# Performance work log

Hardware: AMD Instinct MI355X
Metric: run time of the kernel (lower is better)

The kernel has to match this reference:

```python
import jax, jax.numpy as jnp
import numpy as np
from jax import lax

D_MODEL = 1024
D_STATE = 16
D_CONV = 4
D_INNER = 2048  # expand * d_model
DT_RANK = 64    # ceil(d_model / 16)
BATCH = 2
SEQ = 2048


def setup_inputs() -> dict:
    key = jax.random.key(0)
    ks = jax.random.split(key, 8)
    s = 0.02
    x = jax.random.normal(ks[0], (BATCH, SEQ, D_MODEL), jnp.float32)
    in_proj_w = jax.random.normal(ks[1], (2 * D_INNER, D_MODEL), jnp.float32) * s
    conv_w = jax.random.normal(ks[2], (D_INNER, 1, D_CONV), jnp.float32) * s  # [out, in/groups, k]
    conv_b = jax.random.normal(ks[3], (D_INNER,), jnp.float32) * s
    x_proj_w = jax.random.normal(ks[4], (DT_RANK + 2 * D_STATE, D_INNER), jnp.float32) * s
    dt_proj_w = jax.random.normal(ks[5], (D_INNER, DT_RANK), jnp.float32) * s
    dt_proj_b = jax.random.normal(ks[6], (D_INNER,), jnp.float32) * s
    A_log = jnp.log(jnp.tile(jnp.arange(1, D_STATE + 1, dtype=jnp.float32), (D_INNER, 1)))
    D = jnp.ones((D_INNER,), jnp.float32)
    out_proj_w = jax.random.normal(ks[7], (D_MODEL, D_INNER), jnp.float32) * s
    return dict(x=x, in_proj_w=in_proj_w, conv_w=conv_w, conv_b=conv_b,
                x_proj_w=x_proj_w, dt_proj_w=dt_proj_w, dt_proj_b=dt_proj_b,
                A_log=A_log, D=D, out_proj_w=out_proj_w)


def _causal_depthwise_conv(x_bcl, conv_w, conv_b):
    # x_bcl: [B, d_inner, L]; conv_w: [d_inner, 1, k]; left-pad k-1 -> causal, output length L
    y = lax.conv_general_dilated(
        x_bcl, conv_w,
        window_strides=(1,), padding=[(D_CONV - 1, 0)],
        feature_group_count=D_INNER,
        dimension_numbers=('NCH', 'OIH', 'NCH'))
    return y + conv_b[None, :, None]


def _ssm(xc, x_proj_w, dt_proj_w, dt_proj_b, A_log, D):
    # xc: [B, L, d_inner]
    A = -jnp.exp(A_log)                                   # [d, N]
    x_dbl = jnp.einsum('bld,rd->blr', xc, x_proj_w)       # [B, L, dt_rank + 2N]
    dt_low = x_dbl[..., :DT_RANK]
    Bm = x_dbl[..., DT_RANK:DT_RANK + D_STATE]            # [B, L, N]
    Cm = x_dbl[..., DT_RANK + D_STATE:]                   # [B, L, N]
    dt = jax.nn.softplus(jnp.einsum('blr,dr->bld', dt_low, dt_proj_w) + dt_proj_b)  # [B, L, d]
    dA = jnp.exp(dt[..., None] * A)                       # [B, L, d, N]
    dBx = dt[..., None] * Bm[:, :, None, :] * xc[..., None]  # [B, L, d, N]

    def step(h, inp):
        dA_t, dBx_t, C_t = inp                            # [B,d,N], [B,d,N], [B,N]
        h = dA_t * h + dBx_t
        y = jnp.einsum('bdn,bn->bd', h, C_t)
        return h, y

    h0 = jnp.zeros((xc.shape[0], D_INNER, D_STATE), xc.dtype)
    _, ys = lax.scan(step, h0,
                     (dA.transpose(1, 0, 2, 3), dBx.transpose(1, 0, 2, 3), Cm.transpose(1, 0, 2)))
    y = ys.transpose(1, 0, 2)                             # [B, L, d]
    return y + xc * D


def reference(x, in_proj_w, conv_w, conv_b, x_proj_w, dt_proj_w, dt_proj_b, A_log, D, out_proj_w):
    xz = jnp.einsum('blm,om->blo', x, in_proj_w)          # [B, L, 2*d_inner]
    xs, z = jnp.split(xz, 2, axis=-1)
    xc = _causal_depthwise_conv(xs.transpose(0, 2, 1), conv_w, conv_b).transpose(0, 2, 1)
    xc = jax.nn.silu(xc)
    y = _ssm(xc, x_proj_w, dt_proj_w, dt_proj_b, A_log, D)
    out = y * jax.nn.silu(z)
    return jnp.einsum('bld,md->blm', out, out_proj_w)
```

## Files before the change

### kernel.cpp

```cpp
#include <hip/hip_runtime.h>

#define SEQ    2048
#define DIN    2048
#define DMODEL 1024
#define NROWS  4096
#define NCH    32
#define CHL    64

typedef __attribute__((ext_vector_type(8))) _Float16 half8v;
typedef __attribute__((ext_vector_type(4))) float f32x4;

__device__ __forceinline__ float sigf(float x) { return 1.0f / (1.0f + __expf(-x)); }
__device__ __forceinline__ float softplusf(float v) {
    return fmaxf(v, 0.f) + __logf(1.f + __expf(-fabsf(v)));
}

__device__ __forceinline__ float* deadp(float* xzbuf, size_t j) {
    return xzbuf + ((j >> 11) << 12) + (j & 2047);
}
__device__ __forceinline__ float* deadp2(float* xzbuf, size_t j) {
    return xzbuf + ((size_t)(2048 + (j >> 11)) << 12) + (j & 2047);
}

__device__ __forceinline__ void gload16(const void* g, const void* l) {
    __builtin_amdgcn_global_load_lds((const __attribute__((address_space(1))) void*)g,
                                     (__attribute__((address_space(3))) void*)l, 16, 0, 0);
}

__device__ __forceinline__ unsigned short f2h(float x) {
    _Float16 h = (_Float16)x;
    unsigned short u;
    __builtin_memcpy(&u, &h, 2);
    return u;
}
__device__ __forceinline__ float h2f(unsigned short u) {
    _Float16 h;
    __builtin_memcpy(&h, &u, 2);
    return (float)h;
}

__global__ __launch_bounds__(256) void cvt_in_k(
    const float* __restrict__ x, const float* __restrict__ wi, const float* __restrict__ wx,
    unsigned short* __restrict__ xh, unsigned short* __restrict__ wih,
    unsigned short* __restrict__ wxh)
{
    int i = blockIdx.x * 256 + threadIdx.x;
    if (i < 1048576) {
        float4 v = ((const float4*)x)[i];
        ushort4 h; h.x = f2h(v.x); h.y = f2h(v.y); h.z = f2h(v.z); h.w = f2h(v.w);
        ((ushort4*)xh)[i] = h;
    } else if (i < 2097152) {
        i -= 1048576;
        float4 v = ((const float4*)wi)[i];
        ushort4 h; h.x = f2h(v.x); h.y = f2h(v.y); h.z = f2h(v.z); h.w = f2h(v.w);
        ((ushort4*)wih)[i] = h;
    } else if (i < 2162688) {
        i -= 2097152;
        int row = i >> 9, q = i & 511;
        ushort4 h;
        if (row < 96) {
            float4 v = ((const float4*)wx)[(size_t)row * 512 + q];
            h.x = f2h(v.x); h.y = f2h(v.y); h.z = f2h(v.z); h.w = f2h(v.w);
        } else h = make_ushort4(0, 0, 0, 0);
        ((ushort4*)wxh)[(size_t)row * 512 + q] = h;
    }
}

__global__ __launch_bounds__(256) void cvt_dt_k(
    const float* __restrict__ xdbl, const float* __restrict__ wd, const float* __restrict__ wo,
    unsigned short* __restrict__ dlh, unsigned short* __restrict__ wdh,
    unsigned short* __restrict__ woh)
{
    int i = blockIdx.x * 256 + threadIdx.x;
    if (i < 65536) {
        int row = i >> 4, q = i & 15;
        float4 v = *(const float4*)(xdbl + (size_t)row * 96 + q * 4);
        ushort4 h; h.x = f2h(v.x); h.y = f2h(v.y); h.z = f2h(v.z); h.w = f2h(v.w);
        *(ushort4*)(dlh + (size_t)row * 8192 + q * 4) = h;
    } else if (i < 98304) {
        i -= 65536;
        int row = i >> 4, q = i & 15;
        float4 v = *(const float4*)(wd + (size_t)row * 64 + q * 4);
        ushort4 h; h.x = f2h(v.x); h.y = f2h(v.y); h.z = f2h(v.z); h.w = f2h(v.w);
        *(ushort4*)(wdh + (size_t)row * 8192 + q * 4) = h;
    } else if (i < 622592) {
        i -= 98304;
        float4 v = ((const float4*)wo)[i];
        ushort4 h; h.x = f2h(v.x); h.y = f2h(v.y); h.z = f2h(v.z); h.w = f2h(v.w);
        ((ushort4*)woh)[i] = h;
    }
}

__global__ __launch_bounds__(512, 2) void gemm256_h(
    const unsigned short* __restrict__ A, const unsigned short* __restrict__ W,
    float* __restrict__ C, int K, int N, int mtiles, int lda, int ldw)
{
    __shared__ uint4 ldsu4[8192];
    char* lds = (char*)ldsu4;
    const int tid = threadIdx.x;
    const int w = tid >> 6, lane = tid & 63;

    const int nwg = gridDim.x;
    const int cpx = nwg >> 3;
    const int bid = blockIdx.x;
    const int swz = (bid & 7) * cpx + (bid >> 3);
    const int ntiles = nwg / mtiles;
    const int per = 8 * ntiles;
    const int gid = swz / per;
    const int rem = swz - gid * per;
    const int m0 = (gid * 8 + (rem & 7)) * 256;
    const int n0 = (rem >> 3) * 256;

    const int wr = w >> 2, wc = w & 3;
    const int lm = lane & 15, lk = lane >> 4;

    f32x4 acc[8][4];
#pragma unroll
    for (int i = 0; i < 8; ++i)
#pragma unroll
        for (int j = 0; j < 4; ++j) { acc[i][j][0]=0.f; acc[i][j][1]=0.f; acc[i][j][2]=0.f; acc[i][j][3]=0.f; }

    const int rsub = w * 8 + (lane >> 3);
    const int xr8  = ((lane & 7) ^ (lane >> 3)) << 3;
    const unsigned short* gA = A + (size_t)(m0 + rsub) * lda + xr8;
    const unsigned short* gW = W + (size_t)(n0 + rsub) * ldw + xr8;
    const int sdst = w * 1024;

    auto stageA = [&](int bb, int hi, int kt) {
        char* d = lds + bb * 65536 + hi * 16384 + sdst;
        const unsigned short* s = gA + (size_t)hi * 128 * lda + kt;
        gload16(s, d);
        gload16(s + (size_t)64 * lda, d + 8192);
    };
    auto stageB = [&](int bb, int hi, int kt) {
        char* d = lds + bb * 65536 + 32768 + hi * 16384 + sdst;
        const unsigned short* s = gW + (size_t)hi * 128 * ldw + kt;
        gload16(s, d);
        gload16(s + (size_t)64 * ldw, d + 8192);
    };

    half8v a[4][2], b[2][2][2];
    auto loadA = [&](int bb, int mh) {
#pragma unroll
        for (int mb = 0; mb < 4; ++mb)
#pragma unroll
            for (int kk = 0; kk < 2; ++kk) {
                int ar = wr * 128 + (mh * 4 + mb) * 16 + lm;
                a[mb][kk] = *(const half8v*)(lds + bb * 65536 + ar * 128 + (((kk * 4 + lk) ^ (lm & 7)) << 4));
            }
    };
    auto loadB = [&](int bb, int nh) {
#pragma unroll
        for (int nb = 0; nb < 2; ++nb)
#pragma unroll
            for (int kk = 0; kk < 2; ++kk) {
                int br = wc * 64 + (nh * 2 + nb) * 16 + lm;
                b[nh][nb][kk] = *(const half8v*)(lds + bb * 65536 + 32768 + br * 128 + (((kk * 4 + lk) ^ (lm & 7)) << 4));
            }
    };
    auto mm = [&](int mh, int nh) {
        __builtin_amdgcn_s_setprio(1);
#pragma unroll
        for (int mb = 0; mb < 4; ++mb)
#pragma unroll
            for (int nb = 0; nb < 2; ++nb)
#pragma unroll
                for (int kk = 0; kk < 2; ++kk)
                    acc[mh * 4 + mb][nh * 2 + nb] = __builtin_amdgcn_mfma_f32_16x16x32_f16(
                        a[mb][kk], b[nh][nb][kk], acc[mh * 4 + mb][nh * 2 + nb], 0, 0, 0);
        __builtin_amdgcn_s_setprio(0);
    };
#define VMW4() asm volatile("s_waitcnt vmcnt(4)" ::: "memory")
#define BAR()  __builtin_amdgcn_s_barrier()

    stageA(0, 0, 0); stageA(0, 1, 0); stageB(0, 0, 0); stageB(0, 1, 0);
    asm volatile("s_waitcnt vmcnt(0)" ::: "memory");
    BAR();

    const int NT = K >> 6;
    for (int t = 0; t < NT - 1; ++t) {
        const int cur = t & 1, nxt = cur ^ 1;
        const int kt = (t + 1) << 6;
        loadA(cur, 0); loadB(cur, 0);
        stageA(nxt, 0, kt);
        BAR();
        mm(0, 0);
        VMW4(); BAR();
        loadB(cur, 1);
        stageB(nxt, 0, kt);
        BAR();
        mm(0, 1);
        VMW4(); BAR();
        loadA(cur, 1);
        stageB(nxt, 1, kt);
        BAR();
        mm(1, 1);
        VMW4(); BAR();
        stageA(nxt, 1, kt);
        BAR();
        mm(1, 0);
        VMW4(); BAR();
    }
    {
        const int cur = (NT - 1) & 1;
        asm volatile("s_waitcnt vmcnt(0)" ::: "memory");
        BAR();
        loadA(cur, 0); loadB(cur, 0); mm(0, 0);
        loadB(cur, 1); mm(0, 1);
        loadA(cur, 1); mm(1, 1); mm(1, 0);
    }
#undef VMW4
#undef BAR

#pragma unroll
    for (int mb = 0; mb < 8; ++mb)
#pragma unroll
        for (int nb = 0; nb < 4; ++nb)
#pragma unroll
            for (int r = 0; r < 4; ++r)
                C[(size_t)(m0 + wr * 128 + mb * 16 + lk * 4 + r) * N + (n0 + wc * 64 + nb * 16 + lm)] = acc[mb][nb][r];
}

#define A_OFF 0
#define W_OFF 16384

__global__ __launch_bounds__(256) void gemm_mfma_h(
    const unsigned short* __restrict__ A, const unsigned short* __restrict__ W,
    float* __restrict__ C, int K, int ldc, int nmax, int mtiles, int sA1, int sA2, int ldw,
    const float* __restrict__ bias, int kspl, int cstride)
{
    __shared__ uint4 ldsu4[2048];
    char* lds = (char*)ldsu4;
    const int tid  = threadIdx.x;
    const int w    = tid >> 6, lane = tid & 63;

    const int nwg = gridDim.x;
    const int cpx = nwg >> 3;
    const int bid = blockIdx.x;
    const int swz = (bid & 7) * cpx + (bid >> 3);
    const int nbp = nwg / kspl;
    const int ks  = swz / nbp;
    const int tt  = swz - ks * nbp;
    const int ntiles = nbp / mtiles;
    const int per = 8 * ntiles;
    const int gid = tt / per;
    const int rem = tt - gid * per;
    const int m0 = (gid * 8 + (rem & 7)) * 128;
    const int n0 = (rem >> 3) * 128;
    const int kOff = ks * K;

    const int wr = w >> 1, wc = w & 1;

    f32x4 acc[4][4];
#pragma unroll
    for (int i = 0; i < 4; ++i)
#pragma unroll
        for (int j = 0; j < 4; ++j) { acc[i][j][0]=0.f; acc[i][j][1]=0.f; acc[i][j][2]=0.f; acc[i][j][3]=0.f; }

    const int rloc = w * 32 + (lane >> 3);
    const int xr8  = ((lane & 7) ^ (lane >> 3)) << 3;
    const int rowA = m0 + rloc;
    const unsigned short* gA = A + (size_t)(rowA >> 1) * sA2 + (size_t)(rowA & 1) * sA1 + kOff + xr8;
    const unsigned short* gW = W + (size_t)(n0 + rloc) * ldw + kOff + xr8;

    const int lm  = lane & 15;
    const int lk  = lane >> 4;
    const int lk4 = lk * 4;

    for (int kt = 0; kt < K; kt += 64) {
#pragma unroll
        for (int i = 0; i < 4; ++i) {
            const int rb = w * 32 + i * 8;
            gload16(gA + (size_t)i * 4 * sA2 + kt, lds + A_OFF + rb * 128);
            gload16(gW + (size_t)i * 8 * ldw + kt, lds + W_OFF + rb * 128);
        }
        __syncthreads();
#pragma unroll
        for (int h = 0; h < 2; ++h) {
            half8v af[4], wf[4];
            const int ch = h * 4 + lk;
#pragma unroll
            for (int t = 0; t < 4; ++t) {
                const int ar = wr * 64 + t * 16 + lm;
                const int wrw = wc * 64 + t * 16 + lm;
                af[t] = *(const half8v*)(lds + A_OFF + ar * 128 + ((ch ^ (ar & 7)) << 4));
                wf[t] = *(const half8v*)(lds + W_OFF + wrw * 128 + ((ch ^ (wrw & 7)) << 4));
            }
#pragma unroll
            for (int i = 0; i < 4; ++i)
#pragma unroll
                for (int j = 0; j < 4; ++j)
                    acc[i][j] = __builtin_amdgcn_mfma_f32_16x16x32_f16(af[i], wf[j], acc[i][j], 0, 0, 0);
        }
        __syncthreads();
    }

    float* Cp = C + (size_t)ks * cstride;
    if (bias) {
#pragma unroll
        for (int j = 0; j < 4; ++j) {
            const int n = n0 + wc * 64 + j * 16 + lm;
            const float bv = (n < nmax) ? bias[n] : 0.f;
#pragma unroll
            for (int i = 0; i < 4; ++i)
#pragma unroll
                for (int r = 0; r < 4; ++r) {
                    float v = acc[i][j][r] + bv;
                    if (n < nmax)
                        Cp[(size_t)(m0 + wr * 64 + i * 16 + lk4 + r) * ldc + n] = softplusf(v);
                }
        }
    } else {
#pragma unroll
        for (int i = 0; i < 4; ++i)
#pragma unroll
            for (int j = 0; j < 4; ++j) {
                const int n = n0 + wc * 64 + j * 16 + lm;
                if (n < nmax)
#pragma unroll
                    for (int r = 0; r < 4; ++r)
                        Cp[(size_t)(m0 + wr * 64 + i * 16 + lk4 + r) * ldc + n] = acc[i][j][r];
            }
    }
}

__global__ __launch_bounds__(256) void xproj_reduce_k(
    const float* __restrict__ part, float* __restrict__ xdbl)
{
    int i = blockIdx.x * 256 + threadIdx.x;
    if (i >= NROWS * 24) return;
    int row = i / 24, q = i - row * 24;
    float4 s = make_float4(0.f, 0.f, 0.f, 0.f);
#pragma unroll
    for (int ks = 0; ks < 8; ++ks) {
        float4 v = *(const float4*)(part + (size_t)ks * (NROWS * 128) + (size_t)row * 128 + q * 4);
        s.x += v.x; s.y += v.y; s.z += v.z; s.w += v.w;
    }
    *(float4*)(xdbl + (size_t)row * 96 + q * 4) = s;
}

__global__ __launch_bounds__(256) void out_reduce_k(
    const float* __restrict__ p, float* __restrict__ out)
{
    int i = blockIdx.x * 256 + threadIdx.x;
    float4 a = ((const float4*)p)[i];
    float4 b = ((const float4*)(p + 4194304))[i];
    a.x += b.x; a.y += b.y; a.z += b.z; a.w += b.w;
    ((float4*)out)[i] = a;
}

__global__ __launch_bounds__(256) void conv_silu_k(
    const float* __restrict__ xz, const float* __restrict__ cw,
    const float* __restrict__ cb, unsigned short* __restrict__ xch)
{
    int i = blockIdx.x * 256 + threadIdx.x;
    int d4 = (i & 511) << 2;
    int row = i >> 9;
    int l = row & (SEQ - 1);
    const float* base = xz + (size_t)row * 4096 + d4;
    float4 x0 = *(const float4*)base;
    float4 x1 = (l >= 1) ? *(const float4*)(base - 4096) : make_float4(0, 0, 0, 0);
    float4 x2 = (l >= 2) ? *(const float4*)(base - 8192) : make_float4(0, 0, 0, 0);
    float4 x3 = (l >= 3) ? *(const float4*)(base - 12288) : make_float4(0, 0, 0, 0);
    float4 bv = *(const float4*)(cb + d4);
    ushort4 out;
    unsigned short* op = (unsigned short*)&out;
#pragma unroll
    for (int j = 0; j < 4; ++j) {
        float4 wv = *(const float4*)(cw + (size_t)(d4 + j) * 4);
        float a = ((const float*)&bv)[j];
        a = fmaf(((const float*)&x3)[j], wv.x, a);
        a = fmaf(((const float*)&x2)[j], wv.y, a);
        a = fmaf(((const float*)&x1)[j], wv.z, a);
        a = fmaf(((const float*)&x0)[j], wv.w, a);
        op[j] = f2h(a * sigf(a));
    }
    *(ushort4*)(xch + (size_t)row * DIN + d4) = out;
}

__global__ __launch_bounds__(256) void scan_pass1(
    const float* __restrict__ dt, const unsigned short* __restrict__ xch,
    const float* __restrict__ xdbl, const float* __restrict__ Alog,
    float* __restrict__ xzbuf)
{
    const int b = blockIdx.z, c = blockIdx.y;
    const int d = blockIdx.x * 256 + threadIdx.x;
    float A[16];
#pragma unroll
    for (int q = 0; q < 4; ++q) *(float4*)&A[q * 4] = *(const float4*)&Alog[(size_t)d * 16 + q * 4];
#pragma unroll
    for (int n = 0; n < 16; ++n) A[n] = -__expf(A[n]);
    float h[16] = {}, ap[16];
#pragma unroll
    for (int n = 0; n < 16; ++n) ap[n] = 1.f;
    const int rowbase = b * SEQ + c * CHL;
    for (int t = 0; t < CHL; ++t) {
        const int row = rowbase + t;
        const float* xr = xdbl + (size_t)row * 96;
        float dtv = dt[(size_t)row * DIN + d];
        float xcv = h2f(xch[(size_t)row * DIN + d]);
        float u = dtv * xcv;
#pragma unroll
        for (int n = 0; n < 16; ++n) {
            float dA = __expf(dtv * A[n]);
            h[n] = fmaf(dA, h[n], u * xr[64 + n]);
            ap[n] *= dA;
        }
    }
    size_t e = ((size_t)(b * NCH + c) << 15) + (size_t)d * 16;
#pragma unroll
    for (int q = 0; q < 4; ++q) {
        *(float4*)deadp(xzbuf, e + q * 4)  = *(float4*)&h[q * 4];
        *(float4*)deadp2(xzbuf, e + q * 4) = *(float4*)&ap[q * 4];
    }
}

__global__ __launch_bounds__(256) void scan_pass2(float* __restrict__ xzbuf)
{
    int idx = blockIdx.x * 256 + threadIdx.x;
    int b = idx >> 15;
    int dn = idx & 32767;
    float carry = 0.f;
    for (int c = 0; c < NCH; ++c) {
        size_t e = ((size_t)(b * NCH + c) << 15) + dn;
        float* hp = deadp(xzbuf, e);
        float hl = *hp;
        float ap = *deadp2(xzbuf, e);
        *hp = carry;
        carry = fmaf(ap, carry, hl);
    }
}

__global__ __launch_bounds__(256) void scan_pass3(
    const float* __restrict__ dt, const unsigned short* __restrict__ xch,
    const float* __restrict__ xz, const float* __restrict__ xdbl,
    const float* __restrict__ Alog, const float* __restrict__ Dp,
    float* __restrict__ xzbuf, unsigned short* __restrict__ oph)
{
    const int b = blockIdx.z, c = blockIdx.y;
    const int d = blockIdx.x * 256 + threadIdx.x;
    float A[16];
#pragma unroll
    for (int q = 0; q < 4; ++q) *(float4*)&A[q * 4] = *(const float4*)&Alog[(size_t)d * 16 + q * 4];
#pragma unroll
    for (int n = 0; n < 16; ++n) A[n] = -__expf(A[n]);
    float h[16];
    size_t e = ((size_t)(b * NCH + c) << 15) + (size_t)d * 16;
#pragma unroll
    for (int q = 0; q < 4; ++q) *(float4*)&h[q * 4] = *(float4*)deadp(xzbuf, e + q * 4);
    const float Dd = Dp[d];
    const int rowbase = b * SEQ + c * CHL;
    for (int t = 0; t < CHL; ++t) {
        const int row = rowbase + t;
        const float* xr = xdbl + (size_t)row * 96;
        float dtv = dt[(size_t)row * DIN + d];
        float xcv = h2f(xch[(size_t)row * DIN + d]);
        float zv  = xz[(size_t)row * 4096 + DIN + d];
        float u = dtv * xcv;
        float y = 0.f;
#pragma unroll
        for (int n = 0; n < 16; ++n) {
            float dA = __expf(dtv * A[n]);
            h[n] = fmaf(dA, h[n], u * xr[64 + n]);
            y = fmaf(h[n], xr[80 + n], y);
        }
        float val = (y + xcv * Dd) * zv * sigf(zv);
        oph[(size_t)(row >> 1) * 8192 + (size_t)(row & 1) * 2048 + d] = f2h(val);
    }
}

extern "C" void kernel_launch(void* const* d_in, const int* in_sizes, int n_in,
                              void* d_out, int out_size, void* d_ws, size_t ws_size,
                              hipStream_t stream)
{
    const float* x    = (const float*)d_in[0];
    const float* wi   = (const float*)d_in[1];
    const float* cw   = (const float*)d_in[2];
    const float* cb   = (const float*)d_in[3];
    const float* wx   = (const float*)d_in[4];
    const float* wd   = (const float*)d_in[5];
    const float* bd   = (const float*)d_in[6];
    const float* alog = (const float*)d_in[7];
    const float* Dp   = (const float*)d_in[8];
    const float* wo   = (const float*)d_in[9];
    float* out = (float*)d_out;

    float* wsf  = (float*)d_ws;
    float* xz   = wsf;
    float* xc   = xz + (size_t)NROWS * 4096;
    float* xdbl = xc + (size_t)NROWS * DIN;
    float* dt   = xdbl + (size_t)NROWS * 96;

    unsigned short* xzU = (unsigned short*)xz;
    unsigned short* xh  = (unsigned short*)xc;
    unsigned short* wih = (unsigned short*)dt;
    unsigned short* wxh = (unsigned short*)dt + 4194304;
    unsigned short* xch = (unsigned short*)xc;
    unsigned short* woh = (unsigned short*)xc + 12582912;
    unsigned short* dlh = xzU + 0;
    unsigned short* wdh = xzU + 64;
    unsigned short* oph = xzU + (size_t)2048 * 8192;
    float* xpart = dt + 4194304;
    float* opart = dt;

    cvt_in_k<<<8448, 256, 0, stream>>>(x, wi, wx, xh, wih, wxh);
    gemm256_h<<<256, 512, 0, stream>>>(xh, wih, xz, 1024, 4096, 16, 1024, 1024);
    conv_silu_k<<<8192, 256, 0, stream>>>(xz, cw, cb, xch);
    gemm_mfma_h<<<256, 256, 0, stream>>>(xch, wxh, xpart, 256, 128, 128, 32, 2048, 4096, 2048,
                                         nullptr, 8, NROWS * 128);
    xproj_reduce_k<<<384, 256, 0, stream>>>(xpart, xdbl);
    cvt_dt_k<<<2432, 256, 0, stream>>>(xdbl, wd, wo, dlh, wdh, woh);
    gemm_mfma_h<<<512, 256, 0, stream>>>(dlh, wdh, dt, 64, 2048, 2048, 32, 8192, 16384, 8192,
                                         bd, 1, 0);
    scan_pass1<<<dim3(8, NCH, 2), 256, 0, stream>>>(dt, xch, xdbl, alog, xz);
    scan_pass2<<<256, 256, 0, stream>>>(xz);
    scan_pass3<<<dim3(8, NCH, 2), 256, 0, stream>>>(dt, xch, xz, xdbl, alog, Dp, xz, oph);
    gemm_mfma_h<<<512, 256, 0, stream>>>(oph, woh, opart, 1024, 1024, 1024, 32, 2048, 8192, 2048,
                                         nullptr, 2, 4194304);
    out_reduce_k<<<4096, 256, 0, stream>>>(opart, out);
}
```

Before: 227.2 us.

## Store in_proj output as fp16 and fold dt conversion into reduce

The in_proj GEMM now writes its 4096-wide xz output as fp16 rather than fp32. This halves that intermediate's write traffic and its reads in conv_silu and scan_pass3, and conv_silu now processes 8 channels per thread. The separate cvt_dt_k launch is removed: dt_low is converted to fp16 inside xproj_reduce_k, and the dt_proj and out_proj weight conversions move into the initial cvt kernel. The workspace layout is reorganised with dedicated h/ap scan buffers and compact strides, at the cost of rounding xz and z to fp16 before conv and gating.

```diff
diff --git a/kernel.cpp b/kernel.cpp
--- a/kernel.cpp
+++ b/kernel.cpp
@@ -8,18 +8,12 @@
 #define CHL    64
 
 typedef __attribute__((ext_vector_type(8))) _Float16 half8v;
+typedef __attribute__((ext_vector_type(8))) unsigned short ushort8v;
 typedef __attribute__((ext_vector_type(4))) float f32x4;
 
 __device__ __forceinline__ float sigf(float x) { return 1.0f / (1.0f + __expf(-x)); }
 __device__ __forceinline__ float softplusf(float v) {
     return fmaxf(v, 0.f) + __logf(1.f + __expf(-fabsf(v)));
-}
-
-__device__ __forceinline__ float* deadp(float* xzbuf, size_t j) {
-    return xzbuf + ((j >> 11) << 12) + (j & 2047);
-}
-__device__ __forceinline__ float* deadp2(float* xzbuf, size_t j) {
-    return xzbuf + ((size_t)(2048 + (j >> 11)) << 12) + (j & 2047);
 }
 
 __device__ __forceinline__ void gload16(const void* g, const void* l) {
@@ -41,8 +35,10 @@
 
 __global__ __launch_bounds__(256) void cvt_in_k(
     const float* __restrict__ x, const float* __restrict__ wi, const float* __restrict__ wx,
+    const float* __restrict__ wd, const float* __restrict__ wo,
     unsigned short* __restrict__ xh, unsigned short* __restrict__ wih,
-    unsigned short* __restrict__ wxh)
+    unsigned short* __restrict__ wxh, unsigned short* __restrict__ wdh,
+    unsigned short* __restrict__ woh)
 {
     int i = blockIdx.x * 256 + threadIdx.x;
     if (i < 1048576) {
@@ -63,28 +59,13 @@
             h.x = f2h(v.x); h.y = f2h(v.y); h.z = f2h(v.z); h.w = f2h(v.w);
         } else h = make_ushort4(0, 0, 0, 0);
         ((ushort4*)wxh)[(size_t)row * 512 + q] = h;
-    }
-}
-
-__global__ __launch_bounds__(256) void cvt_dt_k(
-    const float* __restrict__ xdbl, const float* __restrict__ wd, const float* __restrict__ wo,
-    unsigned short* __restrict__ dlh, unsigned short* __restrict__ wdh,
-    unsigned short* __restrict__ woh)
-{
-    int i = blockIdx.x * 256 + threadIdx.x;
-    if (i < 65536) {
-        int row = i >> 4, q = i & 15;
-        float4 v = *(const float4*)(xdbl + (size_t)row * 96 + q * 4);
+    } else if (i < 2195456) {
+        i -= 2162688;
+        float4 v = ((const float4*)wd)[i];
         ushort4 h; h.x = f2h(v.x); h.y = f2h(v.y); h.z = f2h(v.z); h.w = f2h(v.w);
-        *(ushort4*)(dlh + (size_t)row * 8192 + q * 4) = h;
-    } else if (i < 98304) {
-        i -= 65536;
-        int row = i >> 4, q = i & 15;
-        float4 v = *(const float4*)(wd + (size_t)row * 64 + q * 4);
-        ushort4 h; h.x = f2h(v.x); h.y = f2h(v.y); h.z = f2h(v.z); h.w = f2h(v.w);
-        *(ushort4*)(wdh + (size_t)row * 8192 + q * 4) = h;
-    } else if (i < 622592) {
-        i -= 98304;
+        ((ushort4*)wdh)[i] = h;
+    } else {
+        i -= 2195456;
         float4 v = ((const float4*)wo)[i];
         ushort4 h; h.x = f2h(v.x); h.y = f2h(v.y); h.z = f2h(v.z); h.w = f2h(v.w);
         ((ushort4*)woh)[i] = h;
@@ -93,7 +74,7 @@
 
 __global__ __launch_bounds__(512, 2) void gemm256_h(
     const unsigned short* __restrict__ A, const unsigned short* __restrict__ W,
-    float* __restrict__ C, int K, int N, int mtiles, int lda, int ldw)
+    unsigned short* __restrict__ C, int K, int N, int mtiles, int lda, int ldw)
 {
     __shared__ uint4 ldsu4[8192];
     char* lds = (char*)ldsu4;
@@ -218,7 +199,8 @@
         for (int nb = 0; nb < 4; ++nb)
 #pragma unroll
             for (int r = 0; r < 4; ++r)
-                C[(size_t)(m0 + wr * 128 + mb * 16 + lk * 4 + r) * N + (n0 + wc * 64 + nb * 16 + lm)] = acc[mb][nb][r];
+                C[(size_t)(m0 + wr * 128 + mb * 16 + lk * 4 + r) * N + (n0 + wc * 64 + nb * 16 + lm)]
+                    = f2h(acc[mb][nb][r]);
 }
 
 #define A_OFF 0
@@ -325,7 +307,7 @@
 }
 
 __global__ __launch_bounds__(256) void xproj_reduce_k(
-    const float* __restrict__ part, float* __restrict__ xdbl)
+    const float* __restrict__ part, float* __restrict__ xdbl, unsigned short* __restrict__ dlh)
 {
     int i = blockIdx.x * 256 + threadIdx.x;
     if (i >= NROWS * 24) return;
@@ -336,7 +318,12 @@
         float4 v = *(const float4*)(part + (size_t)ks * (NROWS * 128) + (size_t)row * 128 + q * 4);
         s.x += v.x; s.y += v.y; s.z += v.z; s.w += v.w;
     }
-    *(float4*)(xdbl + (size_t)row * 96 + q * 4) = s;
+    if (q < 16) {
+        ushort4 h; h.x = f2h(s.x); h.y = f2h(s.y); h.z = f2h(s.z); h.w = f2h(s.w);
+        *(ushort4*)(dlh + (size_t)row * 64 + q * 4) = h;
+    } else {
+        *(float4*)(xdbl + (size_t)row * 96 + q * 4) = s;
+    }
 }
 
 __global__ __launch_bounds__(256) void out_reduce_k(
@@ -350,38 +337,37 @@
 }
 
 __global__ __launch_bounds__(256) void conv_silu_k(
-    const float* __restrict__ xz, const float* __restrict__ cw,
+    const unsigned short* __restrict__ xzh, const float* __restrict__ cw,
     const float* __restrict__ cb, unsigned short* __restrict__ xch)
 {
     int i = blockIdx.x * 256 + threadIdx.x;
-    int d4 = (i & 511) << 2;
-    int row = i >> 9;
+    int d8 = (i & 255) << 3;
+    int row = i >> 8;
     int l = row & (SEQ - 1);
-    const float* base = xz + (size_t)row * 4096 + d4;
-    float4 x0 = *(const float4*)base;
-    float4 x1 = (l >= 1) ? *(const float4*)(base - 4096) : make_float4(0, 0, 0, 0);
-    float4 x2 = (l >= 2) ? *(const float4*)(base - 8192) : make_float4(0, 0, 0, 0);
-    float4 x3 = (l >= 3) ? *(const float4*)(base - 12288) : make_float4(0, 0, 0, 0);
-    float4 bv = *(const float4*)(cb + d4);
-    ushort4 out;
-    unsigned short* op = (unsigned short*)&out;
-#pragma unroll
-    for (int j = 0; j < 4; ++j) {
-        float4 wv = *(const float4*)(cw + (size_t)(d4 + j) * 4);
-        float a = ((const float*)&bv)[j];
-        a = fmaf(((const float*)&x3)[j], wv.x, a);
-        a = fmaf(((const float*)&x2)[j], wv.y, a);
-        a = fmaf(((const float*)&x1)[j], wv.z, a);
-        a = fmaf(((const float*)&x0)[j], wv.w, a);
-        op[j] = f2h(a * sigf(a));
-    }
-    *(ushort4*)(xch + (size_t)row * DIN + d4) = out;
+    const unsigned short* base = xzh + (size_t)row * 4096 + d8;
+    ushort8v x0 = *(const ushort8v*)base;
+    ushort8v x1 = {}, x2 = {}, x3 = {};
+    if (l >= 1) x1 = *(const ushort8v*)(base - 4096);
+    if (l >= 2) x2 = *(const ushort8v*)(base - 8192);
+    if (l >= 3) x3 = *(const ushort8v*)(base - 12288);
+    ushort8v out;
+#pragma unroll
+    for (int j = 0; j < 8; ++j) {
+        float4 wv = *(const float4*)(cw + (size_t)(d8 + j) * 4);
+        float a = cb[d8 + j];
+        a = fmaf(h2f(x3[j]), wv.x, a);
+        a = fmaf(h2f(x2[j]), wv.y, a);
+        a = fmaf(h2f(x1[j]), wv.z, a);
+        a = fmaf(h2f(x0[j]), wv.w, a);
+        out[j] = f2h(a * sigf(a));
+    }
+    *(ushort8v*)(xch + (size_t)row * DIN + d8) = out;
 }
 
 __global__ __launch_bounds__(256) void scan_pass1(
     const float* __restrict__ dt, const unsigned short* __restrict__ xch,
     const float* __restrict__ xdbl, const float* __restrict__ Alog,
-    float* __restrict__ xzbuf)
+    float* __restrict__ hbuf, float* __restrict__ apbuf)
 {
     const int b = blockIdx.z, c = blockIdx.y;
     const int d = blockIdx.x * 256 + threadIdx.x;
@@ -410,12 +396,13 @@
     size_t e = ((size_t)(b * NCH + c) << 15) + (size_t)d * 16;
 #pragma unroll
     for (int q = 0; q < 4; ++q) {
-        *(float4*)deadp(xzbuf, e + q * 4)  = *(float4*)&h[q * 4];
-        *(float4*)deadp2(xzbuf, e + q * 4) = *(float4*)&ap[q * 4];
-    }
-}
-
-__global__ __launch_bounds__(256) void scan_pass2(float* __restrict__ xzbuf)
+        *(float4*)(hbuf + e + q * 4)  = *(float4*)&h[q * 4];
+        *(float4*)(apbuf + e + q * 4) = *(float4*)&ap[q * 4];
+    }
+}
+
+__global__ __launch_bounds__(256) void scan_pass2(
+    float* __restrict__ hbuf, const float* __restrict__ apbuf)
 {
     int idx = blockIdx.x * 256 + threadIdx.x;
     int b = idx >> 15;
@@ -423,19 +410,18 @@
     float carry = 0.f;
     for (int c = 0; c < NCH; ++c) {
         size_t e = ((size_t)(b * NCH + c) << 15) + dn;
-        float* hp = deadp(xzbuf, e);
-        float hl = *hp;
-        float ap = *deadp2(xzbuf, e);
-        *hp = carry;
+        float hl = hbuf[e];
+        float ap = apbuf[e];
+        hbuf[e] = carry;
         carry = fmaf(ap, carry, hl);
     }
 }
 
 __global__ __launch_bounds__(256) void scan_pass3(
     const float* __restrict__ dt, const unsigned short* __restrict__ xch,
-    const float* __restrict__ xz, const float* __restrict__ xdbl,
+    const unsigned short* __restrict__ xzh, const float* __restrict__ xdbl,
     const float* __restrict__ Alog, const float* __restrict__ Dp,
-    float* __restrict__ xzbuf, unsigned short* __restrict__ oph)
+    const float* __restrict__ hbuf, unsigned short* __restrict__ oph)
 {
     const int b = blockIdx.z, c = blockIdx.y;
     const int d = blockIdx.x * 256 + threadIdx.x;
@@ -447,7 +433,7 @@
     float h[16];
     size_t e = ((size_t)(b * NCH + c) << 15) + (size_t)d * 16;
 #pragma unroll
-    for (int q = 0; q < 4; ++q) *(float4*)&h[q * 4] = *(float4*)deadp(xzbuf, e + q * 4);
+    for (int q = 0; q < 4; ++q) *(float4*)&h[q * 4] = *(const float4*)(hbuf + e + q * 4);
     const float Dd = Dp[d];
     const int rowbase = b * SEQ + c * CHL;
     for (int t = 0; t < CHL; ++t) {
@@ -455,7 +441,7 @@
         const float* xr = xdbl + (size_t)row * 96;
         float dtv = dt[(size_t)row * DIN + d];
         float xcv = h2f(xch[(size_t)row * DIN + d]);
-        float zv  = xz[(size_t)row * 4096 + DIN + d];
+        float zv  = h2f(xzh[(size_t)row * 4096 + DIN + d]);
         float u = dtv * xcv;
         float y = 0.f;
 #pragma unroll
@@ -465,7 +451,7 @@
             y = fmaf(h[n], xr[80 + n], y);
         }
         float val = (y + xcv * Dd) * zv * sigf(zv);
-        oph[(size_t)(row >> 1) * 8192 + (size_t)(row & 1) * 2048 + d] = f2h(val);
+        oph[(size_t)row * DIN + d] = f2h(val);
     }
 }
 
@@ -486,36 +472,40 @@
     float* out = (float*)d_out;
 
     float* wsf  = (float*)d_ws;
-    float* xz   = wsf;
-    float* xc   = xz + (size_t)NROWS * 4096;
-    float* xdbl = xc + (size_t)NROWS * DIN;
-    float* dt   = xdbl + (size_t)NROWS * 96;
-
-    unsigned short* xzU = (unsigned short*)xz;
-    unsigned short* xh  = (unsigned short*)xc;
+    float* xzr  = wsf;
+    float* xcr  = wsf + 16777216;
+    float* xdbl = wsf + 25165824;
+    float* dt   = wsf + 25559040;
+
+    unsigned short* xzh = (unsigned short*)xzr;
+    float* scr = xzr + 8388608;
+    unsigned short* oph = (unsigned short*)scr;
+    float* hbuf         = scr + 4194304;
+    unsigned short* dlh = (unsigned short*)(scr + 6291456);
+    unsigned short* wdh = (unsigned short*)(scr + 6422528);
+    unsigned short* woh = (unsigned short*)(scr + 6488064);
+
+    unsigned short* xh  = (unsigned short*)xcr;
+    unsigned short* xch = (unsigned short*)xcr;
+    float* apbuf        = xcr + 4194304;
+
     unsigned short* wih = (unsigned short*)dt;
     unsigned short* wxh = (unsigned short*)dt + 4194304;
-    unsigned short* xch = (unsigned short*)xc;
-    unsigned short* woh = (unsigned short*)xc + 12582912;
-    unsigned short* dlh = xzU + 0;
-    unsigned short* wdh = xzU + 64;
-    unsigned short* oph = xzU + (size_t)2048 * 8192;
     float* xpart = dt + 4194304;
     float* opart = dt;
 
-    cvt_in_k<<<8448, 256, 0, stream>>>(x, wi, wx, xh, wih, wxh);
-    gemm256_h<<<256, 512, 0, stream>>>(xh, wih, xz, 1024, 4096, 16, 1024, 1024);
-    conv_silu_k<<<8192, 256, 0, stream>>>(xz, cw, cb, xch);
+    cvt_in_k<<<10624, 256, 0, stream>>>(x, wi, wx, wd, wo, xh, wih, wxh, wdh, woh);
+    gemm256_h<<<256, 512, 0, stream>>>(xh, wih, xzh, 1024, 4096, 16, 1024, 1024);
+    conv_silu_k<<<4096, 256, 0, stream>>>(xzh, cw, cb, xch);
     gemm_mfma_h<<<256, 256, 0, stream>>>(xch, wxh, xpart, 256, 128, 128, 32, 2048, 4096, 2048,
                                          nullptr, 8, NROWS * 128);
-    xproj_reduce_k<<<384, 256, 0, stream>>>(xpart, xdbl);
-    cvt_dt_k<<<2432, 256, 0, stream>>>(xdbl, wd, wo, dlh, wdh, woh);
-    gemm_mfma_h<<<512, 256, 0, stream>>>(dlh, wdh, dt, 64, 2048, 2048, 32, 8192, 16384, 8192,
+    xproj_reduce_k<<<384, 256, 0, stream>>>(xpart, xdbl, dlh);
+    gemm_mfma_h<<<512, 256, 0, stream>>>(dlh, wdh, dt, 64, 2048, 2048, 32, 64, 128, 64,
                                          bd, 1, 0);
-    scan_pass1<<<dim3(8, NCH, 2), 256, 0, stream>>>(dt, xch, xdbl, alog, xz);
-    scan_pass2<<<256, 256, 0, stream>>>(xz);
-    scan_pass3<<<dim3(8, NCH, 2), 256, 0, stream>>>(dt, xch, xz, xdbl, alog, Dp, xz, oph);
-    gemm_mfma_h<<<512, 256, 0, stream>>>(oph, woh, opart, 1024, 1024, 1024, 32, 2048, 8192, 2048,
+    scan_pass1<<<dim3(8, NCH, 2), 256, 0, stream>>>(dt, xch, xdbl, alog, hbuf, apbuf);
+    scan_pass2<<<256, 256, 0, stream>>>(hbuf, apbuf);
+    scan_pass3<<<dim3(8, NCH, 2), 256, 0, stream>>>(dt, xch, xzh, xdbl, alog, Dp, hbuf, oph);
+    gemm_mfma_h<<<512, 256, 0, stream>>>(oph, woh, opart, 1024, 1024, 1024, 32, 2048, 4096, 2048,
                                          nullptr, 2, 4194304);
     out_reduce_k<<<4096, 256, 0, stream>>>(opart, out);
 }
```

Result: faster. 219.4 us (-3.4%).
